# Kernel optimization log

Measured on AMD Instinct MI355X. Metric: run time of the kernel, lower is better.

The kernel has to match this reference:

```python
import jax, jax.numpy as jnp
import numpy as np
from jax import lax

VOCAB = 50000; WD = 50; PD = 5; PV = 201  # pos vocab = 2*100+1
HID = 230; REL = 53; L = 120
BAGS = 512; B = 8; N = BAGS * B; QL = 8; EL = 2


def setup_inputs():
    key = jax.random.key(0)
    k = list(jax.random.split(key, 16))
    ar = jnp.arange(BAGS)
    return {
        "X": jax.random.randint(k[0], (N, L), 0, VOCAB),
        "X_Pos1": jax.random.randint(k[1], (N, L), 0, PV),
        "X_Pos2": jax.random.randint(k[2], (N, L), 0, PV),
        "E1": jax.random.randint(k[3], (BAGS * EL,), 0, VOCAB),
        "E2": jax.random.randint(k[4], (BAGS * EL,), 0, VOCAB),
        "X_Mask": jnp.zeros((N, L), jnp.int32),
        "X_Len": jnp.full((N,), L, jnp.int32),
        "X_Scope": jnp.stack([ar * B, ar * B + B], 1),
        "Scope_ent1": jnp.stack([ar * EL, ar * EL + EL], 1),
        "Scope_ent2": jnp.stack([ar * EL, ar * EL + EL], 1),
        "Q": jax.random.randint(k[5], (BAGS, QL), 0, VOCAB),
        "X_Rel": jax.random.randint(k[6], (BAGS,), 0, REL),
        "W_word": 0.1 * jax.random.normal(k[7], (VOCAB, WD), jnp.float32),
        "W_pos1": 0.1 * jax.random.normal(k[8], (PV, PD), jnp.float32),
        "W_pos2": 0.1 * jax.random.normal(k[9], (PV, PD), jnp.float32),
        "w_s": 0.1 * jax.random.normal(k[10], (WD,), jnp.float32),
        "b_s": jnp.zeros((), jnp.float32),
        "w_q": 0.1 * jax.random.normal(k[11], (WD,), jnp.float32),
        "b_q": jnp.zeros((), jnp.float32),
        "w_sq": 0.1 * jax.random.normal(k[12], (WD,), jnp.float32),
        "b_sq": jnp.zeros((), jnp.float32),
        "conv_W": 0.05 * jax.random.normal(k[13], (3, 3 * WD + 2 * PD, HID), jnp.float32),
        "conv_b": jnp.zeros((HID,), jnp.float32),
        "rel_W": 0.1 * jax.random.normal(k[14], (REL, HID), jnp.float32),
        "rel_b": jnp.zeros((REL,), jnp.float32),
    }


def _forward(X, X_Pos1, X_Pos2, E1, E2, Q, X_Rel,
             W_word, W_pos1, W_pos2, w_s, b_s, w_q, b_q, w_sq, b_sq,
             conv_W, conv_b, rel_W, rel_b):
    s = W_word[X]            # [N, L, WD]
    p1 = W_pos1[X_Pos1]      # [N, L, PD]
    p2 = W_pos2[X_Pos2]
    # query embedding: mean entity-mention embeddings into template slots -4 / -2
    e1 = W_word[E1].reshape(BAGS, EL, WD).mean(1)
    e2 = W_word[E2].reshape(BAGS, EL, WD).mean(1)
    q = W_word[Q].at[:, -4].set(e1).at[:, -2].set(e2)  # [BAGS, QL, WD]
    q = jnp.repeat(q, B, axis=0)                        # [N, QL, WD] per-bag repeat
    # BiDAF-style similarity h[n, l, j]
    sq = jnp.einsum('nld,d,njd->nlj', s, w_sq, q) + b_sq
    h = (s @ w_s + b_s)[:, :, None] + (q @ w_q + b_q)[:, None, :] + sq
    a = jax.nn.softmax(h, axis=2)
    s2q = jnp.einsum('nlj,njd->nld', a, q)              # [N, L, WD]
    b_att = jax.nn.softmax(h.max(axis=2), axis=1)       # [N, L]
    q2s = jnp.einsum('nl,nld->nd', b_att, s)            # [N, WD]
    x = jnp.concatenate([s, s * s2q, s * q2s[:, None, :], p1, p2], -1)  # [N, L, 160]
    # CNN encoder: conv1d k=3 SAME, max-over-time, relu
    y = lax.conv_general_dilated(x, conv_W, (1,), 'SAME',
                                 dimension_numbers=('NWC', 'WIO', 'NWC')) + conv_b
    enc = jax.nn.relu(y.max(axis=1))                    # [N, HID]
    # bag self-attention (dropout disabled, eval mode)
    bag = enc.reshape(BAGS, B, HID)
    att = jax.nn.softmax(jnp.einsum('bnd,bmd->bnm', bag, bag) / np.sqrt(HID).astype(np.float32), axis=-1)
    bag = jnp.einsum('bnm,bmd->bnd', att, bag)
    # sentence attention with gold relation query (training branch)
    relv = rel_W[X_Rel]                                 # [BAGS, HID]
    score = jax.nn.softmax(jnp.einsum('bnd,bd->bn', bag, relv), axis=1)
    rep = jnp.einsum('bn,bnd->bd', score, bag)          # [BAGS, HID]
    return rep @ rel_W.T + rel_b                        # [BAGS, REL]


def reference(X, X_Pos1, X_Pos2, E1, E2, X_Mask, X_Len, X_Scope, Scope_ent1, Scope_ent2, Q, X_Rel,
              W_word, W_pos1, W_pos2, w_s, b_s, w_q, b_q, w_sq, b_sq, conv_W, conv_b, rel_W, rel_b):
    # X_Mask / X_Len are PCNN/RNN-encoder inputs, unused by the CNN path.
    # X_Scope / Scope_ent* encode uniform bags (B=8) and mention spans (EL=2),
    # realized here as static reshapes.
    return _forward(X, X_Pos1, X_Pos2, E1, E2, Q, X_Rel,
                    W_word, W_pos1, W_pos2, w_s, b_s, w_q, b_q, w_sq, b_sq,
                    conv_W, conv_b, rel_W, rel_b)
```

## Files before the change

kernel.cpp:

```cpp
#include <hip/hip_runtime.h>
#include <hip/hip_bf16.h>

#define WD 50
#define PD 5
#define HID 230
#define RELN 53
#define LLEN 120
#define BAGS 512
#define BB 8
#define NSENT 4096
#define QL 8
#define CIN 160
#define KTOT 480
#define XROW 168
#define XROWS 122

typedef __attribute__((ext_vector_type(4))) float f32x4;
typedef __attribute__((ext_vector_type(8))) short short8;

__device__ __forceinline__ float bf2f(short u) {
    union { float f; unsigned int i; } v;
    v.i = ((unsigned int)(unsigned short)u) << 16;
    return v.f;
}
__device__ __forceinline__ short f2bf(float f) {
    union { float f; unsigned int i; } v; v.f = f;
    unsigned int r = v.i + 0x7FFFu + ((v.i >> 16) & 1u);
    return (short)(r >> 16);
}

__global__ void build_q_kernel(const int* __restrict__ Q, const int* __restrict__ E1,
                               const int* __restrict__ E2, const float* __restrict__ W_word,
                               float* __restrict__ q_ws) {
    int b = blockIdx.x;
    int d = threadIdx.x;
    if (d >= WD) return;
    float e1 = 0.5f * (W_word[E1[2 * b] * WD + d] + W_word[E1[2 * b + 1] * WD + d]);
    float e2 = 0.5f * (W_word[E2[2 * b] * WD + d] + W_word[E2[2 * b + 1] * WD + d]);
    for (int j = 0; j < QL; ++j) {
        float v;
        if (j == QL - 4)      v = e1;
        else if (j == QL - 2) v = e2;
        else                  v = W_word[Q[b * QL + j] * WD + d];
        q_ws[(b * QL + j) * WD + d] = v;
    }
}

__global__ void pack_w_kernel(const float* __restrict__ conv_W, short* __restrict__ wt2) {
    int i = blockIdx.x * 256 + threadIdx.x;
    if (i >= 15 * 256 * 32) return;
    int ks = i >> 13, rem = i & 8191;
    int row = rem >> 5, kk = rem & 31;
    int k = ks * 32 + kk;
    float v = (row < HID) ? conv_W[k * HID + row] : 0.f;
    wt2[i] = f2bf(v);
}

__launch_bounds__(512, 6)
__global__ void sent_kernel(const int* __restrict__ X, const int* __restrict__ XP1,
                            const int* __restrict__ XP2,
                            const float* __restrict__ W_word,
                            const float* __restrict__ W_pos1, const float* __restrict__ W_pos2,
                            const float* __restrict__ w_s, const float* __restrict__ b_s,
                            const float* __restrict__ w_q, const float* __restrict__ b_q,
                            const float* __restrict__ w_sq, const float* __restrict__ b_sq,
                            const float* __restrict__ conv_b,
                            const float* __restrict__ q_ws, const short* __restrict__ wt2,
                            float* __restrict__ enc) {
    extern __shared__ char smem[];
    short* xl  = (short*)smem;
    short* qtb = xl + XROWS * XROW;
    short* abf = qtb + 64 * 32;
    short* qwb = abf + 136 * 8;
    short* hm  = qwb + 16 * 64;
    float* svv = (float*)(hm + LLEN * 8);
    float* bat = svv + LLEN;
    float* qsv = bat + LLEN;
    float* smax = (float*)qwb;
    float* red  = smax + 512;

    const int tid = threadIdx.x;
    const int n = blockIdx.x;
    const int bag = n >> 3;
    const int lane = tid & 63;
    const int wid = tid >> 6;
    const int r16 = lane & 15;
    const int g = lane >> 4;

    {
        int* xli = (int*)xl;
        for (int i = tid; i < 168; i += 512) {
            int rs = i / 84, col = i % 84;
            int row = (rs == 0) ? 0 : 121;
            xli[row * 84 + col] = 0;
        }
        for (int i = tid; i < 840; i += 512) {
            int row = 1 + i / 7, ci = 25 + i % 7;
            xli[row * 84 + ci] = 0;
        }
        int* abfi = (int*)abf;
        if (tid < 64) abfi[120 * 4 + tid] = 0;
        int* qtbi = (int*)qtb;
        for (int i = tid; i < 1024; i += 512) qtbi[i] = 0;
    }
    if (tid < 480) {
        int l = tid >> 2, q = tid & 3;
        const float* wr = W_word + X[n * LLEN + l] * WD;
        short* dst = xl + (l + 1) * XROW;
        int dp = q * 6;
        int dpe = dp + 6 + (q == 3 ? 1 : 0);
        for (; dp < dpe; ++dp) {
            float2 v = *(const float2*)(wr + dp * 2);
            unsigned int pk = ((unsigned int)(unsigned short)f2bf(v.y) << 16)
                            | (unsigned short)f2bf(v.x);
            *(unsigned int*)(dst + dp * 2) = pk;
        }
    }
    if (tid < 240) {
        int l = tid >> 1, hh = tid & 1;
        const int idx = (hh ? XP2 : XP1)[n * LLEN + l];
        const float* wp = (hh ? W_pos2 : W_pos1) + idx * PD;
        short* dst = xl + (l + 1) * XROW + 150 + hh * PD;
        for (int c = 0; c < PD; ++c) dst[c] = f2bf(wp[c]);
    }
    __syncthreads();
    if (tid < WD) {
        short8 v;
        for (int j = 0; j < QL; ++j) v[j] = f2bf(q_ws[(bag * QL + j) * WD + tid]);
        *(short8*)(qtb + tid * 32) = v;
    }
    if (tid >= 64 && tid < 64 + 72) {
        int t = tid - 64, j = t >> 3, g8 = t & 7;
        short8 v;
        for (int e = 0; e < 8; ++e) {
            int c = g8 * 8 + e;
            float x = 0.f;
            if (c < WD) x = (j < 8) ? q_ws[(bag * QL + j) * WD + c] * w_sq[c] : w_s[c];
            v[e] = f2bf(x);
        }
        *(short8*)(qwb + j * 64 + g8 * 8) = v;
    }
    if (tid >= 504) {
        int j = tid - 504;
        float acc = b_q[0];
        for (int d = 0; d < WD; ++d) acc += q_ws[(bag * QL + j) * WD + d] * w_q[d];
        qsv[j] = acc;
    }
    __syncthreads();

    {
        const float bsq = b_sq[0], bs = b_s[0];
        f32x4 hacc = (f32x4){0.f, 0.f, 0.f, 0.f};
        for (int ks2 = 0; ks2 < 2; ++ks2) {
            short8 af = *(const short8*)(xl + (1 + 16 * wid + r16) * XROW + ks2 * 32 + g * 8);
            short8 bf = *(const short8*)(qwb + r16 * 64 + ks2 * 32 + g * 8);
            hacc = __builtin_amdgcn_mfma_f32_16x16x32_bf16(af, bf, hacc, 0, 0, 0);
        }
        if (r16 < QL) {
            float qs = qsv[r16] + bsq;
            for (int r = 0; r < 4; ++r) {
                int l = 16 * wid + 4 * g + r;
                if (l < LLEN) hm[l * 8 + r16] = f2bf(hacc[r] + qs);
            }
        } else if (r16 == QL) {
            for (int r = 0; r < 4; ++r) {
                int l = 16 * wid + 4 * g + r;
                if (l < LLEN) svv[l] = hacc[r] + bs;
            }
        }
    }
    __syncthreads();

    if (tid < LLEN) {
        const int l = tid;
        short8 hrow = *(const short8*)(hm + l * 8);
        float a[8], m = -1e30f;
        for (int j = 0; j < 8; ++j) { a[j] = bf2f(hrow[j]); m = fmaxf(m, a[j]); }
        float sum = 0.f;
        for (int j = 0; j < 8; ++j) { a[j] = expf(a[j] - m); sum += a[j]; }
        float inv = 1.f / sum;
        short8 arow;
        for (int j = 0; j < 8; ++j) arow[j] = f2bf(a[j] * inv);
        *(short8*)(abf + l * 8) = arow;
        bat[l] = expf(m + svv[l]);
    }
    __syncthreads();

    if (tid < 400) {
        int c = tid / WD, d = tid % WD;
        float acc = 0.f;
        for (int l = c * 15; l < c * 15 + 15; ++l)
            acc += bat[l] * bf2f(xl[(l + 1) * XROW + d]);
        smax[c * 52 + d] = acc;
    } else if (tid >= 448) {
        int ln = tid - 448;
        float v = (ln < LLEN ? bat[ln] : 0.f) + (ln + 64 < LLEN ? bat[ln + 64] : 0.f);
        for (int o = 32; o >= 1; o >>= 1) v += __shfl_xor(v, o, 64);
        if (ln == 0) red[0] = v;
    }
    __syncthreads();

    {
        float rinv = 1.0f / red[0];
        short8 af = *(const short8*)(abf + (16 * wid + r16) * 8 + g * 8);
        for (int nt = 0; nt < 4; ++nt) {
            short8 bf = *(const short8*)(qtb + (16 * nt + r16) * 32 + g * 8);
            f32x4 acc2 = __builtin_amdgcn_mfma_f32_16x16x32_bf16(
                af, bf, (f32x4){0.f, 0.f, 0.f, 0.f}, 0, 0, 0);
            int d = 16 * nt + r16;
            if (d < WD) {
                float q2sd = 0.f;
                for (int c = 0; c < 8; ++c) q2sd += smax[c * 52 + d];
                q2sd *= rinv;
                for (int r = 0; r < 4; ++r) {
                    int l = 16 * wid + 4 * g + r;
                    if (l < LLEN) {
                        short* row = xl + (l + 1) * XROW;
                        float s = bf2f(row[d]);
                        row[50 + d]  = f2bf(s * acc2[r]);
                        row[100 + d] = f2bf(s * q2sd);
                    }
                }
            }
        }
    }
    __syncthreads();

    const int wm = wid >> 2;
    const int wn = wid & 3;
    const int m0 = 64 * wm + r16;
    const short* wbase = wt2 + (64 * wn + r16) * 32 + g * 8;
    const int aoff_base = m0 * XROW + g * 8;

#pragma unroll 1
    for (int p = 0; p < 2; ++p) {
        f32x4 acc[4][2];
        for (int a = 0; a < 4; ++a) {
            acc[a][0] = (f32x4){0.f, 0.f, 0.f, 0.f};
            acc[a][1] = (f32x4){0.f, 0.f, 0.f, 0.f};
        }
        const short* wb = wbase + p * 1024;
        short8 b0[2], b1[2];
        b0[0] = *(const short8*)(wb);
        b0[1] = *(const short8*)(wb + 512);
        int aoff = aoff_base;

#pragma unroll 1
        for (int ks = 0; ks < 14; ks += 2) {
            const short* wk = wb + ks * 8192;
            b1[0] = *(const short8*)(wk + 8192);
            b1[1] = *(const short8*)(wk + 8192 + 512);
            {
#pragma unroll
                for (int mf = 0; mf < 4; ++mf) {
                    short8 afr = *(const short8*)(xl + aoff + mf * (16 * XROW));
                    acc[mf][0] = __builtin_amdgcn_mfma_f32_16x16x32_bf16(afr, b0[0], acc[mf][0], 0, 0, 0);
                    acc[mf][1] = __builtin_amdgcn_mfma_f32_16x16x32_bf16(afr, b0[1], acc[mf][1], 0, 0, 0);
                }
            }
            b0[0] = *(const short8*)(wk + 16384);
            b0[1] = *(const short8*)(wk + 16384 + 512);
            {
                const int aoff1 = aoff + ((ks == 4) ? 40 : 32);
#pragma unroll
                for (int mf = 0; mf < 4; ++mf) {
                    short8 afr = *(const short8*)(xl + aoff1 + mf * (16 * XROW));
                    acc[mf][0] = __builtin_amdgcn_mfma_f32_16x16x32_bf16(afr, b1[0], acc[mf][0], 0, 0, 0);
                    acc[mf][1] = __builtin_amdgcn_mfma_f32_16x16x32_bf16(afr, b1[1], acc[mf][1], 0, 0, 0);
                }
            }
            aoff += 64 + ((ks == 4 || ks == 8) ? 8 : 0);
        }
        {
#pragma unroll
            for (int mf = 0; mf < 4; ++mf) {
                short8 afr = *(const short8*)(xl + aoff + mf * (16 * XROW));
                acc[mf][0] = __builtin_amdgcn_mfma_f32_16x16x32_bf16(afr, b0[0], acc[mf][0], 0, 0, 0);
                acc[mf][1] = __builtin_amdgcn_mfma_f32_16x16x32_bf16(afr, b0[1], acc[mf][1], 0, 0, 0);
            }
        }
#pragma unroll
        for (int nf = 0; nf < 2; ++nf) {
            float m = -1e30f;
#pragma unroll
            for (int mf = 0; mf < 4; ++mf) {
                int lbase = 64 * wm + 16 * mf + 4 * g;
#pragma unroll
                for (int r = 0; r < 4; ++r)
                    if (lbase + r < LLEN) m = fmaxf(m, acc[mf][nf][r]);
            }
            m = fmaxf(m, __shfl_xor(m, 16, 64));
            m = fmaxf(m, __shfl_xor(m, 32, 64));
            if (lane < 16) smax[wm * 256 + 64 * wn + 32 * p + 16 * nf + r16] = m;
        }
    }
    __syncthreads();
    for (int h = tid; h < HID; h += 512) {
        float v = fmaxf(smax[h], smax[256 + h]) + conv_b[h];
        enc[n * HID + h] = fmaxf(v, 0.f);
    }
}

__global__ void bag_kernel(const float* __restrict__ enc, const int* __restrict__ X_Rel,
                           const float* __restrict__ rel_W, const float* __restrict__ rel_b,
                           float* __restrict__ out) {
    __shared__ float bagv[BB][232];
    __shared__ float bag2[BB][232];
    __shared__ float att[BB][BB];
    __shared__ float relv[232];
    __shared__ float repv[232];
    __shared__ float sc[BB], sc2[BB];
    const int b = blockIdx.x, t = threadIdx.x;

    for (int i = t; i < BB * HID; i += 256) {
        int r = i / HID, d = i % HID;
        bagv[r][d] = enc[(b * BB + r) * HID + d];
    }
    __syncthreads();
    if (t < 64) {
        int i = t >> 3, j = t & 7;
        float acc = 0.f;
        for (int d = 0; d < HID; ++d) acc += bagv[i][d] * bagv[j][d];
        att[i][j] = acc * (1.0f / sqrtf(230.0f));
    }
    __syncthreads();
    if (t < 8) {
        float m = att[t][0];
        for (int j = 1; j < 8; ++j) m = fmaxf(m, att[t][j]);
        float e[8], s = 0.f;
        for (int j = 0; j < 8; ++j) { e[j] = expf(att[t][j] - m); s += e[j]; }
        float inv = 1.f / s;
        for (int j = 0; j < 8; ++j) att[t][j] = e[j] * inv;
    }
    __syncthreads();
    for (int i = t; i < BB * HID; i += 256) {
        int r = i / HID, d = i % HID;
        float acc = 0.f;
        for (int j = 0; j < 8; ++j) acc += att[r][j] * bagv[j][d];
        bag2[r][d] = acc;
    }
    if (t < HID) relv[t] = rel_W[X_Rel[b] * HID + t];
    __syncthreads();
    if (t < 8) {
        float acc = 0.f;
        for (int d = 0; d < HID; ++d) acc += bag2[t][d] * relv[d];
        sc[t] = acc;
    }
    __syncthreads();
    if (t < 8) {
        float m = sc[0];
        for (int j = 1; j < 8; ++j) m = fmaxf(m, sc[j]);
        sc2[t] = expf(sc[t] - m);
    }
    __syncthreads();
    if (t < HID) {
        float sum = 0.f;
        for (int j = 0; j < 8; ++j) sum += sc2[j];
        float acc = 0.f;
        for (int j = 0; j < 8; ++j) acc += sc2[j] * bag2[j][t];
        repv[t] = acc / sum;
    }
    __syncthreads();
    if (t < RELN) {
        float acc = rel_b[t];
        for (int d = 0; d < HID; ++d) acc += repv[d] * rel_W[t * HID + d];
        out[b * RELN + t] = acc;
    }
}

extern "C" void kernel_launch(void* const* d_in, const int* in_sizes, int n_in,
                              void* d_out, int out_size, void* d_ws, size_t ws_size,
                              hipStream_t stream) {
    const int* X       = (const int*)d_in[0];
    const int* XP1     = (const int*)d_in[1];
    const int* XP2     = (const int*)d_in[2];
    const int* E1      = (const int*)d_in[3];
    const int* E2      = (const int*)d_in[4];
    const int* Q       = (const int*)d_in[10];
    const int* X_Rel   = (const int*)d_in[11];
    const float* W_word = (const float*)d_in[12];
    const float* W_pos1 = (const float*)d_in[13];
    const float* W_pos2 = (const float*)d_in[14];
    const float* w_s   = (const float*)d_in[15];
    const float* b_s   = (const float*)d_in[16];
    const float* w_q   = (const float*)d_in[17];
    const float* b_q   = (const float*)d_in[18];
    const float* w_sq  = (const float*)d_in[19];
    const float* b_sq  = (const float*)d_in[20];
    const float* conv_W = (const float*)d_in[21];
    const float* conv_b = (const float*)d_in[22];
    const float* rel_W = (const float*)d_in[23];
    const float* rel_b = (const float*)d_in[24];
    float* out = (float*)d_out;

    char* ws = (char*)d_ws;
    float* q_ws = (float*)ws;
    float* enc  = q_ws + BAGS * QL * WD;
    short* wt2  = (short*)(enc + NSENT * HID);

    build_q_kernel<<<BAGS, 64, 0, stream>>>(Q, E1, E2, W_word, q_ws);
    pack_w_kernel<<<480, 256, 0, stream>>>(conv_W, wt2);

    const size_t lds_bytes =
        (size_t)XROWS * XROW * 2
        + 64 * 32 * 2
        + 136 * 8 * 2
        + 16 * 64 * 2
        + LLEN * 8 * 2
        + 4 * (LLEN + LLEN + 8);
    sent_kernel<<<NSENT, 512, lds_bytes, stream>>>(
        X, XP1, XP2, W_word, W_pos1, W_pos2,
        w_s, b_s, w_q, b_q, w_sq, b_sq, conv_b, q_ws, wt2, enc);

    bag_kernel<<<BAGS, 256, 0, stream>>>(enc, X_Rel, rel_W, rel_b, out);
}
```

Before: 197.2 us.

## Fuse per-token softmax into MFMA epilogue via lane shuffles and drop barriers

Computes the 8-way query softmax and the token attention weight directly from MFMA accumulators using cross-lane shuffles, which removes the hm/svv staging buffers and one block-wide barrier plus a serial pass over 120 tokens. It also moves the query/weight setup work before the first barrier, so one fewer __syncthreads is needed. Float-to-bf16 packing now uses the hardware v_cvt_pk_bf16_f32 instruction, and exp is replaced by the fast __expf intrinsic. Shared memory shrinks slightly. The softmax now runs on fp32 logits instead of bf16-rounded ones, so results change slightly in numerics.

```diff
diff --git a/kernel.cpp b/kernel.cpp
--- a/kernel.cpp
+++ b/kernel.cpp
@@ -27,6 +27,11 @@
     union { float f; unsigned int i; } v; v.f = f;
     unsigned int r = v.i + 0x7FFFu + ((v.i >> 16) & 1u);
     return (short)(r >> 16);
+}
+__device__ __forceinline__ unsigned int cvtpk(float a, float b) {
+    unsigned int r;
+    asm("v_cvt_pk_bf16_f32 %0, %1, %2" : "=v"(r) : "v"(a), "v"(b));
+    return r;
 }
 
 __global__ void build_q_kernel(const int* __restrict__ Q, const int* __restrict__ E1,
@@ -72,12 +77,10 @@
     short* qtb = xl + XROWS * XROW;
     short* abf = qtb + 64 * 32;
     short* qwb = abf + 136 * 8;
-    short* hm  = qwb + 16 * 64;
-    float* svv = (float*)(hm + LLEN * 8);
-    float* bat = svv + LLEN;
-    float* qsv = bat + LLEN;
     float* smax = (float*)qwb;
     float* red  = smax + 512;
+    float* bat  = (float*)((char*)qwb + 2056);
+    float* qsv  = bat + LLEN;
 
     const int tid = threadIdx.x;
     const int n = blockIdx.x;
@@ -90,18 +93,16 @@
     {
         int* xli = (int*)xl;
         for (int i = tid; i < 168; i += 512) {
-            int rs = i / 84, col = i % 84;
-            int row = (rs == 0) ? 0 : 121;
+            int col = (i < 84) ? i : (i - 84);
+            int row = (i < 84) ? 0 : 121;
             xli[row * 84 + col] = 0;
         }
-        for (int i = tid; i < 840; i += 512) {
-            int row = 1 + i / 7, ci = 25 + i % 7;
+        for (int i = tid; i < 960; i += 512) {
+            int row = 1 + (i >> 3), ci = 25 + (i & 7);
             xli[row * 84 + ci] = 0;
         }
         int* abfi = (int*)abf;
         if (tid < 64) abfi[120 * 4 + tid] = 0;
-        int* qtbi = (int*)qtb;
-        for (int i = tid; i < 1024; i += 512) qtbi[i] = 0;
     }
     if (tid < 480) {
         int l = tid >> 2, q = tid & 3;
@@ -111,9 +112,7 @@
         int dpe = dp + 6 + (q == 3 ? 1 : 0);
         for (; dp < dpe; ++dp) {
             float2 v = *(const float2*)(wr + dp * 2);
-            unsigned int pk = ((unsigned int)(unsigned short)f2bf(v.y) << 16)
-                            | (unsigned short)f2bf(v.x);
-            *(unsigned int*)(dst + dp * 2) = pk;
+            *(unsigned int*)(dst + dp * 2) = cvtpk(v.x, v.y);
         }
     }
     if (tid < 240) {
@@ -123,14 +122,20 @@
         short* dst = xl + (l + 1) * XROW + 150 + hh * PD;
         for (int c = 0; c < PD; ++c) dst[c] = f2bf(wp[c]);
     }
-    __syncthreads();
-    if (tid < WD) {
-        short8 v;
-        for (int j = 0; j < QL; ++j) v[j] = f2bf(q_ws[(bag * QL + j) * WD + tid]);
-        *(short8*)(qtb + tid * 32) = v;
-    }
-    if (tid >= 64 && tid < 64 + 72) {
-        int t = tid - 64, j = t >> 3, g8 = t & 7;
+    if (tid >= 448) {
+        int d = tid - 448;
+        short8 v = (short8){0, 0, 0, 0, 0, 0, 0, 0};
+        if (d < WD)
+            for (int j = 0; j < QL; ++j) v[j] = f2bf(q_ws[(bag * QL + j) * WD + d]);
+        short* dst = qtb + d * 32;
+        short8 z = (short8){0, 0, 0, 0, 0, 0, 0, 0};
+        *(short8*)(dst) = v;
+        *(short8*)(dst + 8) = z;
+        *(short8*)(dst + 16) = z;
+        *(short8*)(dst + 24) = z;
+    }
+    if (tid >= 376 && tid < 448) {
+        int t = tid - 376, j = t >> 3, g8 = t & 7;
         short8 v;
         for (int e = 0; e < 8; ++e) {
             int c = g8 * 8 + e;
@@ -140,8 +145,8 @@
         }
         *(short8*)(qwb + j * 64 + g8 * 8) = v;
     }
-    if (tid >= 504) {
-        int j = tid - 504;
+    if (tid >= 368 && tid < 376) {
+        int j = tid - 368;
         float acc = b_q[0];
         for (int d = 0; d < WD; ++d) acc += q_ws[(bag * QL + j) * WD + d] * w_q[d];
         qsv[j] = acc;
@@ -156,33 +161,42 @@
             short8 bf = *(const short8*)(qwb + r16 * 64 + ks2 * 32 + g * 8);
             hacc = __builtin_amdgcn_mfma_f32_16x16x32_bf16(af, bf, hacc, 0, 0, 0);
         }
-        if (r16 < QL) {
-            float qs = qsv[r16] + bsq;
+        const float qs = (r16 < QL) ? (qsv[r16] + bsq) : 0.f;
+        float an[4], mx[4];
+#pragma unroll
+        for (int r = 0; r < 4; ++r) {
+            float h = hacc[r] + qs;
+            float m = h;
+            m = fmaxf(m, __shfl_xor(m, 1, 64));
+            m = fmaxf(m, __shfl_xor(m, 2, 64));
+            m = fmaxf(m, __shfl_xor(m, 4, 64));
+            mx[r] = m;
+            float a = __expf(h - m);
+            float s = a;
+            s += __shfl_xor(s, 1, 64);
+            s += __shfl_xor(s, 2, 64);
+            s += __shfl_xor(s, 4, 64);
+            an[r] = a / s;
+        }
+        unsigned int w[4];
+#pragma unroll
+        for (int r = 0; r < 4; ++r) w[r] = cvtpk(an[r], __shfl_xor(an[r], 1, 64));
+        if (r16 < QL && !(r16 & 1)) {
+#pragma unroll
             for (int r = 0; r < 4; ++r) {
                 int l = 16 * wid + 4 * g + r;
-                if (l < LLEN) hm[l * 8 + r16] = f2bf(hacc[r] + qs);
-            }
-        } else if (r16 == QL) {
+                if (l < LLEN) *(unsigned int*)(abf + l * 8 + r16) = w[r];
+            }
+        }
+#pragma unroll
+        for (int r = 0; r < 4; ++r) mx[r] = __shfl_xor(mx[r], 8, 64);
+        if (r16 == QL) {
+#pragma unroll
             for (int r = 0; r < 4; ++r) {
                 int l = 16 * wid + 4 * g + r;
-                if (l < LLEN) svv[l] = hacc[r] + bs;
-            }
-        }
-    }
-    __syncthreads();
-
-    if (tid < LLEN) {
-        const int l = tid;
-        short8 hrow = *(const short8*)(hm + l * 8);
-        float a[8], m = -1e30f;
-        for (int j = 0; j < 8; ++j) { a[j] = bf2f(hrow[j]); m = fmaxf(m, a[j]); }
-        float sum = 0.f;
-        for (int j = 0; j < 8; ++j) { a[j] = expf(a[j] - m); sum += a[j]; }
-        float inv = 1.f / sum;
-        short8 arow;
-        for (int j = 0; j < 8; ++j) arow[j] = f2bf(a[j] * inv);
-        *(short8*)(abf + l * 8) = arow;
-        bat[l] = expf(m + svv[l]);
+                if (l < LLEN) bat[l] = __expf(mx[r] + hacc[r] + bs);
+            }
+        }
     }
     __syncthreads();
 
@@ -405,9 +419,9 @@
         (size_t)XROWS * XROW * 2
         + 64 * 32 * 2
         + 136 * 8 * 2
-        + 16 * 64 * 2
-        + LLEN * 8 * 2
-        + 4 * (LLEN + LLEN + 8);
+        + 2056
+        + 4 * LLEN
+        + 4 * QL;
     sent_kernel<<<NSENT, 512, lds_bytes, stream>>>(
         X, XP1, XP2, W_word, W_pos1, W_pos2,
         w_s, b_s, w_q, b_q, w_sq, b_sq, conv_b, q_ws, wt2, enc);
```

Measured after the change: 201.7 us. 1.02x slower.
